# Kernel optimization log

Hardware: AMD Instinct MI355X
Metric: run time of the kernel (lower is better)

Reference implementation:

```python
import jax, jax.numpy as jnp
import numpy as np

SCALE_REACH = 10.0   # 'scale' in forward
SCALE_COS = 16.0     # CosNorm_Classifier default scale


def setup_inputs() -> dict:
    key = jax.random.key(0)
    ks = jax.random.split(key, 7)
    B, C, F = 64, 1000, 2048
    return {
        "x": jax.random.normal(ks[0], (B, F), jnp.float32),
        "centroids": jax.random.normal(ks[1], (C, F), jnp.float32),
        "W_hall": jax.random.normal(ks[2], (C, F), jnp.float32) * 0.02,
        "b_hall": jax.random.normal(ks[3], (C,), jnp.float32) * 0.02,
        "W_sel": jax.random.normal(ks[4], (F, F), jnp.float32) * 0.02,
        "b_sel": jax.random.normal(ks[5], (F,), jnp.float32) * 0.02,
        "W_cos": jax.random.normal(ks[6], (C, F), jnp.float32) * 0.001,
    }


def reference(x, centroids, W_hall, b_hall, W_sel, b_sel, W_cos):
    direct_feature = x
    # L2 distance to every class centroid: [B, C] (materializes [B, C, F] diff as in torch)
    diff = x[:, None, :] - centroids[None, :, :]
    dist = jnp.sqrt(jnp.sum(diff * diff, axis=2))
    # original sorts then takes column 0 -> min distance
    min_dist = jnp.min(dist, axis=1)                      # [B]
    reachability = (SCALE_REACH / min_dist)[:, None]      # [B, 1], broadcast over feat

    # hallucinated memory read
    values_memory = jax.nn.softmax(x @ W_hall.T + b_hall, axis=1)  # [B, C]
    memory_feature = values_memory @ centroids                      # [B, F]

    concept_selector = jnp.tanh(x @ W_sel.T + b_sel)                # [B, F]
    infused_feature = concept_selector * memory_feature
    feat = reachability * (direct_feature + infused_feature)

    # CosNorm classifier
    norm_x = jnp.linalg.norm(feat, axis=1, keepdims=True)           # [B, 1]
    ex = (norm_x / (1.0 + norm_x)) * (feat / norm_x)                # norm-gated unit vec
    ew = W_cos / jnp.linalg.norm(W_cos, axis=1, keepdims=True)      # [C, F]
    logits = ex @ (ew.T * SCALE_COS)                                # [B, C]

    return logits, direct_feature, infused_feature
```

## Files before the change

kernel.cpp:

```cpp
#include <hip/hip_runtime.h>
#include <math.h>

#define FF 2048

typedef __attribute__((ext_vector_type(8))) short short8;
typedef __attribute__((ext_vector_type(4))) float floatx4;

#define OFF_SPART 0
#define OFF_HPART 512000
#define OFF_SELP  1024000
#define OFF_MEMP  2072576
#define OFF_LOGP  3121152
#define OFF_V     4145152
#define OFF_FEAT  4210688
#define OFF_CN2   4341760
#define OFF_WINV  4342760
#define OFF_XN2   4343760
#define OFF_REACH 4343824
#define OFF_NRM2P 4343888

#define TP 40

__device__ __forceinline__ void split2(float f, ushort& h, ushort& l) {
  unsigned u = __float_as_uint(f);
  float r = f - __uint_as_float(u & 0xffff0000u);
  h = (ushort)(u >> 16);
  l = (ushort)(__float_as_uint(r) >> 16);
}

__device__ __forceinline__ void stage_bt_bf(const float* __restrict__ M, int ldK, int rowBase,
                                            int nrows, int k0, int kmax,
                                            ushort* __restrict__ hi, ushort* __restrict__ lo, int t) {
  int r = t >> 2, q = t & 3;
  int grow = rowBase + r;
  bool rok = grow < nrows;
  const float* src = M + (size_t)grow * ldK + k0 + q * 8;
#pragma unroll
  for (int h = 0; h < 2; ++h) {
    int kb = k0 + q * 8 + h * 4;
    float4 v = make_float4(0.f, 0.f, 0.f, 0.f);
    if (rok) {
      if (kb + 3 < kmax) {
        v = *(const float4*)(src + h * 4);
      } else {
#pragma unroll
        for (int j = 0; j < 4; ++j)
          if (kb + j < kmax) ((float*)&v)[j] = src[h * 4 + j];
      }
    }
    ushort4 hv, lv;
    split2(v.x, hv.x, lv.x); split2(v.y, hv.y, lv.y);
    split2(v.z, hv.z, lv.z); split2(v.w, hv.w, lv.w);
    int base = r * TP + q * 8 + h * 4;
    *(ushort4*)(hi + base) = hv;
    *(ushort4*)(lo + base) = lv;
  }
}

__device__ __forceinline__ void stage_tr_bf(const float* __restrict__ M, int ldN, int k0, int kmax,
                                            int n0, ushort* __restrict__ hi, ushort* __restrict__ lo, int t) {
  int kk = t >> 3, c8 = (t & 7) * 8;
  int gk = k0 + kk;
  const float* src = M + (size_t)gk * ldN + n0 + c8;
  float4 v0 = make_float4(0.f, 0.f, 0.f, 0.f), v1 = v0;
  if (gk < kmax) { v0 = *(const float4*)src; v1 = *(const float4*)(src + 4); }
#pragma unroll
  for (int j = 0; j < 8; ++j) {
    float f = (j < 4) ? ((float*)&v0)[j] : ((float*)&v1)[j - 4];
    ushort h, l;
    split2(f, h, l);
    hi[(c8 + j) * TP + kk] = h;
    lo[(c8 + j) * TP + kk] = l;
  }
}

#define MFMA(a, b, c) __builtin_amdgcn_mfma_f32_16x16x32_bf16(a, b, c, 0, 0, 0)

__global__ __launch_bounds__(256) void ka_gemm1(
    const float* __restrict__ x, const float* __restrict__ cent,
    const float* __restrict__ whall, const float* __restrict__ wsel,
    const float* __restrict__ wcos, float* __restrict__ ws) {
  __shared__ __align__(16) ushort u_lds[6 * 64 * TP];
  ushort* Ah  = u_lds;
  ushort* Al  = u_lds + 64 * TP;
  ushort* B1h = u_lds + 2 * 64 * TP;
  ushort* B1l = u_lds + 3 * 64 * TP;
  ushort* B2h = u_lds + 4 * 64 * TP;
  ushort* B2l = u_lds + 5 * 64 * TP;
  int bx = blockIdx.x, t = threadIdx.x;
  int lane = t & 63, w = t >> 6;
  int ln15 = t & 15, lq = (t >> 4) & 3, q8 = lq * 8;
  int mh = w & 1, nh = w >> 1;

  for (int r = bx * 4 + w; r < 2064; r += 2048) {
    const float* src = (r < 1000) ? cent + (size_t)r * FF
                     : (r < 2000) ? wcos + (size_t)(r - 1000) * FF
                                  : x + (size_t)(r - 2000) * FF;
    float s = 0.f;
#pragma unroll
    for (int i = 0; i < 8; ++i) {
      float4 v = *(const float4*)(src + i * 256 + lane * 4);
      s += v.x * v.x + v.y * v.y + v.z * v.z + v.w * v.w;
    }
#pragma unroll
    for (int off = 32; off > 0; off >>= 1) s += __shfl_down(s, off, 64);
    if (lane == 0) {
      if (r < 1000) ws[OFF_CN2 + r] = s;
      else if (r < 2000) ws[OFF_WINV + (r - 1000)] = 1.f / sqrtf(s);
      else ws[OFF_XN2 + (r - 2000)] = s;
    }
  }

  if (bx < 128) {
    int tile = bx & 15, ks = bx >> 4;
    int n0 = tile * 64;
    floatx4 accS[2][2], accH[2][2];
#pragma unroll
    for (int i = 0; i < 2; ++i)
#pragma unroll
      for (int j = 0; j < 2; ++j) { accS[i][j] = (floatx4){0.f,0.f,0.f,0.f}; accH[i][j] = (floatx4){0.f,0.f,0.f,0.f}; }
    for (int kc = 0; kc < 8; ++kc) {
      int k0 = ks * 256 + kc * 32;
      __syncthreads();
      stage_bt_bf(x,     FF, 0,  64,   k0, FF, Ah,  Al,  t);
      stage_bt_bf(cent,  FF, n0, 1000, k0, FF, B1h, B1l, t);
      stage_bt_bf(whall, FF, n0, 1000, k0, FF, B2h, B2l, t);
      __syncthreads();
      short8 ah[2], al[2];
#pragma unroll
      for (int i = 0; i < 2; ++i) {
        int row = (mh * 2 + i) * 16 + ln15;
        ah[i] = *(const short8*)(Ah + row * TP + q8);
        al[i] = *(const short8*)(Al + row * TP + q8);
      }
#pragma unroll
      for (int j = 0; j < 2; ++j) {
        int brow = (nh * 2 + j) * 16 + ln15;
        short8 b1h = *(const short8*)(B1h + brow * TP + q8);
        short8 b1l = *(const short8*)(B1l + brow * TP + q8);
        short8 b2h = *(const short8*)(B2h + brow * TP + q8);
        short8 b2l = *(const short8*)(B2l + brow * TP + q8);
#pragma unroll
        for (int i = 0; i < 2; ++i) {
          accS[i][j] = MFMA(ah[i], b1h, accS[i][j]);
          accS[i][j] = MFMA(ah[i], b1l, accS[i][j]);
          accS[i][j] = MFMA(al[i], b1h, accS[i][j]);
          accH[i][j] = MFMA(ah[i], b2h, accH[i][j]);
          accH[i][j] = MFMA(ah[i], b2l, accH[i][j]);
          accH[i][j] = MFMA(al[i], b2h, accH[i][j]);
        }
      }
    }
    float* Spart = ws + OFF_SPART + (size_t)ks * 64000;
    float* Hpart = ws + OFF_HPART + (size_t)ks * 64000;
#pragma unroll
    for (int i = 0; i < 2; ++i)
#pragma unroll
      for (int j = 0; j < 2; ++j) {
        int gn = n0 + (nh * 2 + j) * 16 + ln15;
        if (gn < 1000) {
#pragma unroll
          for (int r = 0; r < 4; ++r) {
            int gm = (mh * 2 + i) * 16 + lq * 4 + r;
            Spart[gm * 1000 + gn] = accS[i][j][r];
            Hpart[gm * 1000 + gn] = accH[i][j][r];
          }
        }
      }
  } else if (bx < 384) {
    int b2 = bx - 128;
    int tile = b2 & 31, ks = b2 >> 5;
    int n0 = tile * 64;
    floatx4 acc[2][2];
#pragma unroll
    for (int i = 0; i < 2; ++i)
#pragma unroll
      for (int j = 0; j < 2; ++j) acc[i][j] = (floatx4){0.f,0.f,0.f,0.f};
    for (int kc = 0; kc < 8; ++kc) {
      int k0 = ks * 256 + kc * 32;
      __syncthreads();
      stage_bt_bf(x,    FF, 0,  64, k0, FF, Ah,  Al,  t);
      stage_bt_bf(wsel, FF, n0, FF, k0, FF, B1h, B1l, t);
      __syncthreads();
      short8 ah[2], al[2];
#pragma unroll
      for (int i = 0; i < 2; ++i) {
        int row = (mh * 2 + i) * 16 + ln15;
        ah[i] = *(const short8*)(Ah + row * TP + q8);
        al[i] = *(const short8*)(Al + row * TP + q8);
      }
#pragma unroll
      for (int j = 0; j < 2; ++j) {
        int brow = (nh * 2 + j) * 16 + ln15;
        short8 bh = *(const short8*)(B1h + brow * TP + q8);
        short8 bl = *(const short8*)(B1l + brow * TP + q8);
#pragma unroll
        for (int i = 0; i < 2; ++i) {
          acc[i][j] = MFMA(ah[i], bh, acc[i][j]);
          acc[i][j] = MFMA(ah[i], bl, acc[i][j]);
          acc[i][j] = MFMA(al[i], bh, acc[i][j]);
        }
      }
    }
    float* selp = ws + OFF_SELP + (size_t)ks * 131072;
#pragma unroll
    for (int i = 0; i < 2; ++i)
#pragma unroll
      for (int j = 0; j < 2; ++j) {
        int gn = n0 + (nh * 2 + j) * 16 + ln15;
#pragma unroll
        for (int r = 0; r < 4; ++r) {
          int gm = (mh * 2 + i) * 16 + lq * 4 + r;
          selp[gm * 2048 + gn] = acc[i][j][r];
        }
      }
  }
}

__global__ __launch_bounds__(256) void kb_softmax(const float* __restrict__ bhall,
                                                  float* __restrict__ ws) {
  __shared__ float hrow[1000];
  __shared__ float red[256];
  int b = blockIdx.x, t = threadIdx.x;
  float xn = ws[OFF_XN2 + b];
  float lmin = 3.0e38f, lmax = -3.0e38f;
  if (t < 250) {
    int c0 = t * 4;
    floatx4 S = {0.f,0.f,0.f,0.f}, H = {0.f,0.f,0.f,0.f};
#pragma unroll
    for (int ks = 0; ks < 8; ++ks) {
      floatx4 sv = *(const floatx4*)(ws + OFF_SPART + (size_t)ks * 64000 + b * 1000 + c0);
      floatx4 hv = *(const floatx4*)(ws + OFF_HPART + (size_t)ks * 64000 + b * 1000 + c0);
      S += sv; H += hv;
    }
    floatx4 bh = *(const floatx4*)(bhall + c0);
    floatx4 cn = *(const floatx4*)(ws + OFF_CN2 + c0);
#pragma unroll
    for (int j = 0; j < 4; ++j) {
      float Hf = H[j] + bh[j];
      hrow[c0 + j] = Hf;
      float d2 = xn - 2.f * S[j] + cn[j];
      lmin = fminf(lmin, d2);
      lmax = fmaxf(lmax, Hf);
    }
  }
  red[t] = lmin; __syncthreads();
  for (int s = 128; s > 0; s >>= 1) { if (t < s) red[t] = fminf(red[t], red[t + s]); __syncthreads(); }
  float bmin = red[0]; __syncthreads();
  red[t] = lmax; __syncthreads();
  for (int s = 128; s > 0; s >>= 1) { if (t < s) red[t] = fmaxf(red[t], red[t + s]); __syncthreads(); }
  float bmax = red[0]; __syncthreads();
  float lsum = 0.f;
  float e4[4] = {0.f, 0.f, 0.f, 0.f};
  if (t < 250) {
#pragma unroll
    for (int j = 0; j < 4; ++j) {
      e4[j] = expf(hrow[t * 4 + j] - bmax);
      lsum += e4[j];
    }
  }
  red[t] = lsum; __syncthreads();
  for (int s = 128; s > 0; s >>= 1) { if (t < s) red[t] += red[t + s]; __syncthreads(); }
  float inv = 1.f / red[0];
  if (t < 250)
    *(floatx4*)(ws + OFF_V + b * 1024 + t * 4) =
        (floatx4){e4[0] * inv, e4[1] * inv, e4[2] * inv, e4[3] * inv};
  if (t == 250) {
#pragma unroll
    for (int j = 0; j < 24; ++j) ws[OFF_V + b * 1024 + 1000 + j] = 0.f;
  }
  if (t == 0) ws[OFF_REACH + b] = 10.f / sqrtf(bmin);
}

__global__ __launch_bounds__(256) void kc_mem(const float* __restrict__ cent,
                                              float* __restrict__ ws) {
  __shared__ __align__(16) ushort u_lds[4 * 64 * TP];
  ushort* Ah  = u_lds;
  ushort* Al  = u_lds + 64 * TP;
  ushort* B1h = u_lds + 2 * 64 * TP;
  ushort* B1l = u_lds + 3 * 64 * TP;
  int bx = blockIdx.x, t = threadIdx.x;
  int tile = bx & 31, ks = bx >> 5;
  int n0 = tile * 64;
  int ln15 = t & 15, lq = (t >> 4) & 3, q8 = lq * 8;
  int w = t >> 6, mh = w & 1, nh = w >> 1;
  const float* V = ws + OFF_V;
  floatx4 acc[2][2];
#pragma unroll
  for (int i = 0; i < 2; ++i)
#pragma unroll
    for (int j = 0; j < 2; ++j) acc[i][j] = (floatx4){0.f,0.f,0.f,0.f};
  for (int kc = 0; kc < 4; ++kc) {
    int k0 = ks * 128 + kc * 32;
    __syncthreads();
    {
      int r = t >> 2, q = t & 3;
#pragma unroll
      for (int h = 0; h < 2; ++h) {
        float4 v = *(const float4*)(V + (size_t)r * 1024 + k0 + q * 8 + h * 4);
        ushort4 hv, lv;
        split2(v.x, hv.x, lv.x); split2(v.y, hv.y, lv.y);
        split2(v.z, hv.z, lv.z); split2(v.w, hv.w, lv.w);
        int base = r * TP + q * 8 + h * 4;
        *(ushort4*)(Ah + base) = hv;
        *(ushort4*)(Al + base) = lv;
      }
    }
    stage_tr_bf(cent, FF, k0, 1000, n0, B1h, B1l, t);
    __syncthreads();
    short8 ah[2], al[2];
#pragma unroll
    for (int i = 0; i < 2; ++i) {
      int row = (mh * 2 + i) * 16 + ln15;
      ah[i] = *(const short8*)(Ah + row * TP + q8);
      al[i] = *(const short8*)(Al + row * TP + q8);
    }
#pragma unroll
    for (int j = 0; j < 2; ++j) {
      int brow = (nh * 2 + j) * 16 + ln15;
      short8 bh = *(const short8*)(B1h + brow * TP + q8);
      short8 bl = *(const short8*)(B1l + brow * TP + q8);
#pragma unroll
      for (int i = 0; i < 2; ++i) {
        acc[i][j] = MFMA(ah[i], bh, acc[i][j]);
        acc[i][j] = MFMA(ah[i], bl, acc[i][j]);
        acc[i][j] = MFMA(al[i], bh, acc[i][j]);
      }
    }
  }
  float* memp = ws + OFF_MEMP + (size_t)ks * 131072;
#pragma unroll
  for (int i = 0; i < 2; ++i)
#pragma unroll
    for (int j = 0; j < 2; ++j) {
      int gn = n0 + (nh * 2 + j) * 16 + ln15;
#pragma unroll
      for (int r = 0; r < 4; ++r) {
        int gm = (mh * 2 + i) * 16 + lq * 4 + r;
        memp[gm * 2048 + gn] = acc[i][j][r];
      }
    }
}

__global__ __launch_bounds__(64) void kd_fuse(const float* __restrict__ x,
                                              const float* __restrict__ bsel,
                                              float* __restrict__ ws, float* __restrict__ out) {
  int bx = blockIdx.x, t = threadIdx.x;
  int row = bx >> 3, ch = bx & 7;
  int f = ch * 256 + t * 4;
  const float* selp = ws + OFF_SELP + (size_t)row * 2048 + f;
  const float* memp = ws + OFF_MEMP + (size_t)row * 2048 + f;
  floatx4 sp = {0.f,0.f,0.f,0.f}, mm = {0.f,0.f,0.f,0.f};
#pragma unroll
  for (int ks = 0; ks < 8; ++ks) {
    sp += *(const floatx4*)(selp + (size_t)ks * 131072);
    mm += *(const floatx4*)(memp + (size_t)ks * 131072);
  }
  float4 bs4 = *(const float4*)(bsel + f);
  float4 x4  = *(const float4*)(x + (size_t)row * 2048 + f);
  float rch = ws[OFF_REACH + row];
  float4 inf4;
  floatx4 ft4;
  float nrm2 = 0.f;
#pragma unroll
  for (int j = 0; j < 4; ++j) {
    float sel = tanhf(sp[j] + ((float*)&bs4)[j]);
    float inf = sel * mm[j];
    float ft = rch * (((float*)&x4)[j] + inf);
    ((float*)&inf4)[j] = inf;
    ft4[j] = ft;
    nrm2 += ft * ft;
  }
  *(float4*)(out + 64000 + (size_t)row * 2048 + f) = x4;
  *(float4*)(out + 195072 + (size_t)row * 2048 + f) = inf4;
  *(floatx4*)(ws + OFF_FEAT + (size_t)row * 2048 + f) = ft4;
#pragma unroll
  for (int off = 32; off > 0; off >>= 1) nrm2 += __shfl_down(nrm2, off, 64);
  if (t == 0) ws[OFF_NRM2P + row * 8 + ch] = nrm2;
}

__global__ __launch_bounds__(256) void ke_logits(const float* __restrict__ wcos,
                                                 float* __restrict__ ws) {
  __shared__ __align__(16) ushort u_lds[4 * 64 * TP];
  ushort* Ah  = u_lds;
  ushort* Al  = u_lds + 64 * TP;
  ushort* B1h = u_lds + 2 * 64 * TP;
  ushort* B1l = u_lds + 3 * 64 * TP;
  int bx = blockIdx.x, t = threadIdx.x;
  int tile = bx & 15, ks = bx >> 4;
  int n0 = tile * 64;
  int ln15 = t & 15, lq = (t >> 4) & 3, q8 = lq * 8;
  int w = t >> 6, mh = w & 1, nh = w >> 1;
  const float* feat = ws + OFF_FEAT;
  floatx4 acc[2][2];
#pragma unroll
  for (int i = 0; i < 2; ++i)
#pragma unroll
    for (int j = 0; j < 2; ++j) acc[i][j] = (floatx4){0.f,0.f,0.f,0.f};
  for (int kc = 0; kc < 4; ++kc) {
    int k0 = ks * 128 + kc * 32;
    __syncthreads();
    {
      int r = t >> 2, q = t & 3;
#pragma unroll
      for (int h = 0; h < 2; ++h) {
        float4 v = *(const float4*)(feat + (size_t)r * 2048 + k0 + q * 8 + h * 4);
        ushort4 hv, lv;
        split2(v.x, hv.x, lv.x); split2(v.y, hv.y, lv.y);
        split2(v.z, hv.z, lv.z); split2(v.w, hv.w, lv.w);
        int base = r * TP + q * 8 + h * 4;
        *(ushort4*)(Ah + base) = hv;
        *(ushort4*)(Al + base) = lv;
      }
    }
    stage_bt_bf(wcos, FF, n0, 1000, k0, FF, B1h, B1l, t);
    __syncthreads();
    short8 ah[2], al[2];
#pragma unroll
    for (int i = 0; i < 2; ++i) {
      int row = (mh * 2 + i) * 16 + ln15;
      ah[i] = *(const short8*)(Ah + row * TP + q8);
      al[i] = *(const short8*)(Al + row * TP + q8);
    }
#pragma unroll
    for (int j = 0; j < 2; ++j) {
      int brow = (nh * 2 + j) * 16 + ln15;
      short8 bh = *(const short8*)(B1h + brow * TP + q8);
      short8 bl = *(const short8*)(B1l + brow * TP + q8);
#pragma unroll
      for (int i = 0; i < 2; ++i) {
        acc[i][j] = MFMA(ah[i], bh, acc[i][j]);
        acc[i][j] = MFMA(ah[i], bl, acc[i][j]);
        acc[i][j] = MFMA(al[i], bh, acc[i][j]);
      }
    }
  }
  float* logp = ws + OFF_LOGP + (size_t)ks * 64000;
#pragma unroll
  for (int i = 0; i < 2; ++i)
#pragma unroll
    for (int j = 0; j < 2; ++j) {
      int gn = n0 + (nh * 2 + j) * 16 + ln15;
      if (gn < 1000) {
#pragma unroll
        for (int r = 0; r < 4; ++r) {
          int gm = (mh * 2 + i) * 16 + lq * 4 + r;
          logp[gm * 1000 + gn] = acc[i][j][r];
        }
      }
    }
}

__global__ __launch_bounds__(128) void kf_final(float* __restrict__ ws, float* __restrict__ out) {
  int bx = blockIdx.x, t = threadIdx.x;
  int idx0 = (bx * 128 + t) * 4;
  const float* logp = ws + OFF_LOGP + idx0;
  floatx4 s = {0.f,0.f,0.f,0.f};
#pragma unroll
  for (int ks = 0; ks < 16; ++ks)
    s += *(const floatx4*)(logp + (size_t)ks * 64000);
  floatx4 o4;
  int pb = -1;
  float sfac = 0.f;
#pragma unroll
  for (int j = 0; j < 4; ++j) {
    int idx = idx0 + j;
    int bb = idx / 1000;
    int cc = idx - bb * 1000;
    if (bb != pb) {
      float n2 = 0.f;
#pragma unroll
      for (int q = 0; q < 8; ++q) n2 += ws[OFF_NRM2P + bb * 8 + q];
      sfac = 16.f / (1.f + sqrtf(n2));
      pb = bb;
    }
    o4[j] = s[j] * sfac * ws[OFF_WINV + cc];
  }
  *(floatx4*)(out + idx0) = o4;
}

extern "C" void kernel_launch(void* const* d_in, const int* in_sizes, int n_in,
                              void* d_out, int out_size, void* d_ws, size_t ws_size,
                              hipStream_t stream) {
  const float* x     = (const float*)d_in[0];
  const float* cent  = (const float*)d_in[1];
  const float* whall = (const float*)d_in[2];
  const float* bhall = (const float*)d_in[3];
  const float* wsel  = (const float*)d_in[4];
  const float* bsel  = (const float*)d_in[5];
  const float* wcos  = (const float*)d_in[6];
  float* out = (float*)d_out;
  float* ws  = (float*)d_ws;

  hipLaunchKernelGGL(ka_gemm1,   dim3(512), dim3(256), 0, stream, x, cent, whall, wsel, wcos, ws);
  hipLaunchKernelGGL(kb_softmax, dim3(64),  dim3(256), 0, stream, bhall, ws);
  hipLaunchKernelGGL(kc_mem,     dim3(256), dim3(256), 0, stream, cent, ws);
  hipLaunchKernelGGL(kd_fuse,    dim3(512), dim3(64),  0, stream, x, bsel, ws, out);
  hipLaunchKernelGGL(ke_logits,  dim3(256), dim3(256), 0, stream, wcos, ws);
  hipLaunchKernelGGL(kf_final,   dim3(125), dim3(128), 0, stream, ws, out);
}
```

Measured before the change: 131.6 us.

## Fuse six kernels into one cooperative persistent kernel with grid syncs

Replaces the six separate kernel launches with a single cooperative kernel of 512 blocks that runs every stage and separates them with grid.sync(). The first GEMM stage is rebalanced so each block handles a single B matrix (cent, whall or wsel) instead of some blocks doing two GEMMs at once, which spreads the work over all 512 blocks. This is meant to remove launch gaps and inter-kernel drain, at the cost of grid-wide barriers, idle blocks during the small stages, and the need for all 512 blocks to be co-resident (launch_bounds 256,2).

```diff
diff --git a/kernel.cpp b/kernel.cpp
--- a/kernel.cpp
+++ b/kernel.cpp
@@ -1,5 +1,8 @@
 #include <hip/hip_runtime.h>
+#include <hip/hip_cooperative_groups.h>
 #include <math.h>
+
+namespace cg = cooperative_groups;
 
 #define FF 2048
 
@@ -76,21 +79,22 @@
 
 #define MFMA(a, b, c) __builtin_amdgcn_mfma_f32_16x16x32_bf16(a, b, c, 0, 0, 0)
 
-__global__ __launch_bounds__(256) void ka_gemm1(
+__global__ __launch_bounds__(256, 2) void mega(
     const float* __restrict__ x, const float* __restrict__ cent,
-    const float* __restrict__ whall, const float* __restrict__ wsel,
-    const float* __restrict__ wcos, float* __restrict__ ws) {
-  __shared__ __align__(16) ushort u_lds[6 * 64 * TP];
-  ushort* Ah  = u_lds;
-  ushort* Al  = u_lds + 64 * TP;
-  ushort* B1h = u_lds + 2 * 64 * TP;
-  ushort* B1l = u_lds + 3 * 64 * TP;
-  ushort* B2h = u_lds + 4 * 64 * TP;
-  ushort* B2l = u_lds + 5 * 64 * TP;
-  int bx = blockIdx.x, t = threadIdx.x;
-  int lane = t & 63, w = t >> 6;
-  int ln15 = t & 15, lq = (t >> 4) & 3, q8 = lq * 8;
-  int mh = w & 1, nh = w >> 1;
+    const float* __restrict__ whall, const float* __restrict__ bhall,
+    const float* __restrict__ wsel, const float* __restrict__ bsel,
+    const float* __restrict__ wcos, float* __restrict__ ws,
+    float* __restrict__ out) {
+  cg::grid_group grid = cg::this_grid();
+  __shared__ __align__(16) ushort u_lds[4 * 64 * TP];
+  ushort* Ah = u_lds;
+  ushort* Al = u_lds + 64 * TP;
+  ushort* Bh = u_lds + 2 * 64 * TP;
+  ushort* Bl = u_lds + 3 * 64 * TP;
+  const int bx = blockIdx.x, t = threadIdx.x;
+  const int lane = t & 63, w = t >> 6;
+  const int ln15 = t & 15, lq = (t >> 4) & 3, q8 = lq * 8;
+  const int mh = w & 1, nh = w >> 1;
 
   for (int r = bx * 4 + w; r < 2064; r += 2048) {
     const float* src = (r < 1000) ? cent + (size_t)r * FF
@@ -111,20 +115,24 @@
     }
   }
 
-  if (bx < 128) {
-    int tile = bx & 15, ks = bx >> 4;
-    int n0 = tile * 64;
-    floatx4 accS[2][2], accH[2][2];
-#pragma unroll
-    for (int i = 0; i < 2; ++i)
-#pragma unroll
-      for (int j = 0; j < 2; ++j) { accS[i][j] = (floatx4){0.f,0.f,0.f,0.f}; accH[i][j] = (floatx4){0.f,0.f,0.f,0.f}; }
+  {
+    const int tile = bx & 63, ks = bx >> 6;
+    const float* Bm;
+    float* outp;
+    int n0, nB, ldo;
+    if (tile < 16)      { Bm = cent;  n0 = tile * 64;        nB = 1000; outp = ws + OFF_SPART + (size_t)ks * 64000;  ldo = 1000; }
+    else if (tile < 32) { Bm = whall; n0 = (tile - 16) * 64; nB = 1000; outp = ws + OFF_HPART + (size_t)ks * 64000;  ldo = 1000; }
+    else                { Bm = wsel;  n0 = (tile - 32) * 64; nB = 2048; outp = ws + OFF_SELP  + (size_t)ks * 131072; ldo = 2048; }
+    floatx4 acc[2][2];
+#pragma unroll
+    for (int i = 0; i < 2; ++i)
+#pragma unroll
+      for (int j = 0; j < 2; ++j) acc[i][j] = (floatx4){0.f, 0.f, 0.f, 0.f};
     for (int kc = 0; kc < 8; ++kc) {
       int k0 = ks * 256 + kc * 32;
       __syncthreads();
-      stage_bt_bf(x,     FF, 0,  64,   k0, FF, Ah,  Al,  t);
-      stage_bt_bf(cent,  FF, n0, 1000, k0, FF, B1h, B1l, t);
-      stage_bt_bf(whall, FF, n0, 1000, k0, FF, B2h, B2l, t);
+      stage_bt_bf(x,  FF, 0,  64, k0, FF, Ah, Al, t);
+      stage_bt_bf(Bm, FF, n0, nB, k0, FF, Bh, Bl, t);
       __syncthreads();
       short8 ah[2], al[2];
 #pragma unroll
@@ -136,51 +144,116 @@
 #pragma unroll
       for (int j = 0; j < 2; ++j) {
         int brow = (nh * 2 + j) * 16 + ln15;
-        short8 b1h = *(const short8*)(B1h + brow * TP + q8);
-        short8 b1l = *(const short8*)(B1l + brow * TP + q8);
-        short8 b2h = *(const short8*)(B2h + brow * TP + q8);
-        short8 b2l = *(const short8*)(B2l + brow * TP + q8);
+        short8 bh = *(const short8*)(Bh + brow * TP + q8);
+        short8 bl = *(const short8*)(Bl + brow * TP + q8);
 #pragma unroll
         for (int i = 0; i < 2; ++i) {
-          accS[i][j] = MFMA(ah[i], b1h, accS[i][j]);
-          accS[i][j] = MFMA(ah[i], b1l, accS[i][j]);
-          accS[i][j] = MFMA(al[i], b1h, accS[i][j]);
-          accH[i][j] = MFMA(ah[i], b2h, accH[i][j]);
-          accH[i][j] = MFMA(ah[i], b2l, accH[i][j]);
-          accH[i][j] = MFMA(al[i], b2h, accH[i][j]);
-        }
-      }
-    }
-    float* Spart = ws + OFF_SPART + (size_t)ks * 64000;
-    float* Hpart = ws + OFF_HPART + (size_t)ks * 64000;
+          acc[i][j] = MFMA(ah[i], bh, acc[i][j]);
+          acc[i][j] = MFMA(ah[i], bl, acc[i][j]);
+          acc[i][j] = MFMA(al[i], bh, acc[i][j]);
+        }
+      }
+    }
 #pragma unroll
     for (int i = 0; i < 2; ++i)
 #pragma unroll
       for (int j = 0; j < 2; ++j) {
         int gn = n0 + (nh * 2 + j) * 16 + ln15;
-        if (gn < 1000) {
+        if (gn < nB) {
 #pragma unroll
           for (int r = 0; r < 4; ++r) {
             int gm = (mh * 2 + i) * 16 + lq * 4 + r;
-            Spart[gm * 1000 + gn] = accS[i][j][r];
-            Hpart[gm * 1000 + gn] = accH[i][j][r];
+            outp[gm * ldo + gn] = acc[i][j][r];
           }
         }
       }
-  } else if (bx < 384) {
-    int b2 = bx - 128;
-    int tile = b2 & 31, ks = b2 >> 5;
-    int n0 = tile * 64;
+  }
+
+  grid.sync();
+
+  if (bx < 64) {
+    float* fl = (float*)u_lds;
+    float* hrow = fl;
+    float* red = fl + 1024;
+    int b = bx;
+    float xn = ws[OFF_XN2 + b];
+    float lmin = 3.0e38f, lmax = -3.0e38f;
+    if (t < 250) {
+      int c0 = t * 4;
+      floatx4 S = {0.f, 0.f, 0.f, 0.f}, H = {0.f, 0.f, 0.f, 0.f};
+#pragma unroll
+      for (int ks = 0; ks < 8; ++ks) {
+        floatx4 sv = *(const floatx4*)(ws + OFF_SPART + (size_t)ks * 64000 + b * 1000 + c0);
+        floatx4 hv = *(const floatx4*)(ws + OFF_HPART + (size_t)ks * 64000 + b * 1000 + c0);
+        S += sv; H += hv;
+      }
+      floatx4 bh = *(const floatx4*)(bhall + c0);
+      floatx4 cn = *(const floatx4*)(ws + OFF_CN2 + c0);
+#pragma unroll
+      for (int j = 0; j < 4; ++j) {
+        float Hf = H[j] + bh[j];
+        hrow[c0 + j] = Hf;
+        float d2 = xn - 2.f * S[j] + cn[j];
+        lmin = fminf(lmin, d2);
+        lmax = fmaxf(lmax, Hf);
+      }
+    }
+    red[t] = lmin; __syncthreads();
+    for (int s = 128; s > 0; s >>= 1) { if (t < s) red[t] = fminf(red[t], red[t + s]); __syncthreads(); }
+    float bmin = red[0]; __syncthreads();
+    red[t] = lmax; __syncthreads();
+    for (int s = 128; s > 0; s >>= 1) { if (t < s) red[t] = fmaxf(red[t], red[t + s]); __syncthreads(); }
+    float bmax = red[0]; __syncthreads();
+    float lsum = 0.f;
+    float e4[4] = {0.f, 0.f, 0.f, 0.f};
+    if (t < 250) {
+#pragma unroll
+      for (int j = 0; j < 4; ++j) {
+        e4[j] = expf(hrow[t * 4 + j] - bmax);
+        lsum += e4[j];
+      }
+    }
+    red[t] = lsum; __syncthreads();
+    for (int s = 128; s > 0; s >>= 1) { if (t < s) red[t] += red[t + s]; __syncthreads(); }
+    float inv = 1.f / red[0];
+    if (t < 250)
+      *(floatx4*)(ws + OFF_V + b * 1024 + t * 4) =
+          (floatx4){e4[0] * inv, e4[1] * inv, e4[2] * inv, e4[3] * inv};
+    if (t == 250) {
+#pragma unroll
+      for (int j = 0; j < 24; ++j) ws[OFF_V + b * 1024 + 1000 + j] = 0.f;
+    }
+    if (t == 0) ws[OFF_REACH + b] = 10.f / sqrtf(bmin);
+  }
+
+  grid.sync();
+
+  if (bx < 256) {
+    const int tile = bx & 31, ks = bx >> 5;
+    const int n0 = tile * 64;
+    const float* V = ws + OFF_V;
     floatx4 acc[2][2];
 #pragma unroll
     for (int i = 0; i < 2; ++i)
 #pragma unroll
-      for (int j = 0; j < 2; ++j) acc[i][j] = (floatx4){0.f,0.f,0.f,0.f};
-    for (int kc = 0; kc < 8; ++kc) {
-      int k0 = ks * 256 + kc * 32;
-      __syncthreads();
-      stage_bt_bf(x,    FF, 0,  64, k0, FF, Ah,  Al,  t);
-      stage_bt_bf(wsel, FF, n0, FF, k0, FF, B1h, B1l, t);
+      for (int j = 0; j < 2; ++j) acc[i][j] = (floatx4){0.f, 0.f, 0.f, 0.f};
+    for (int kc = 0; kc < 4; ++kc) {
+      int k0 = ks * 128 + kc * 32;
+      __syncthreads();
+      {
+        int r = t >> 2, q = t & 3;
+#pragma unroll
+        for (int h = 0; h < 2; ++h) {
+          float4 v = *(const float4*)(V + (size_t)r * 1024 + k0 + q * 8 + h * 4);
+          ushort4 hv, lv;
+          split2(v.x, hv.x, lv.x); split2(v.y, hv.y, lv.y);
+          split2(v.z, hv.z, lv.z); split2(v.w, hv.w, lv.w);
+          int base = r * TP + q * 8 + h * 4;
+          *(ushort4*)(Ah + base) = hv;
+          *(ushort4*)(Al + base) = lv;
+        }
+      }
+      stage_tr_bf(cent, FF, k0, 1000, n0, Bh, Bl, t);
       __syncthreads();
       short8 ah[2], al[2];
 #pragma unroll
@@ -192,8 +265,8 @@
 #pragma unroll
       for (int j = 0; j < 2; ++j) {
         int brow = (nh * 2 + j) * 16 + ln15;
-        short8 bh = *(const short8*)(B1h + brow * TP + q8);
-        short8 bl = *(const short8*)(B1l + brow * TP + q8);
+        short8 bh = *(const short8*)(Bh + brow * TP + q8);
+        short8 bl = *(const short8*)(Bl + brow * TP + q8);
 #pragma unroll
         for (int i = 0; i < 2; ++i) {
           acc[i][j] = MFMA(ah[i], bh, acc[i][j]);
@@ -202,7 +275,7 @@
         }
       }
     }
-    float* selp = ws + OFF_SELP + (size_t)ks * 131072;
+    float* memp = ws + OFF_MEMP + (size_t)ks * 131072;
 #pragma unroll
     for (int i = 0; i < 2; ++i)
 #pragma unroll
@@ -211,272 +284,142 @@
 #pragma unroll
         for (int r = 0; r < 4; ++r) {
           int gm = (mh * 2 + i) * 16 + lq * 4 + r;
-          selp[gm * 2048 + gn] = acc[i][j][r];
-        }
-      }
-  }
-}
-
-__global__ __launch_bounds__(256) void kb_softmax(const float* __restrict__ bhall,
-                                                  float* __restrict__ ws) {
-  __shared__ float hrow[1000];
-  __shared__ float red[256];
-  int b = blockIdx.x, t = threadIdx.x;
-  float xn = ws[OFF_XN2 + b];
-  float lmin = 3.0e38f, lmax = -3.0e38f;
-  if (t < 250) {
-    int c0 = t * 4;
-    floatx4 S = {0.f,0.f,0.f,0.f}, H = {0.f,0.f,0.f,0.f};
+          memp[gm * 2048 + gn] = acc[i][j][r];
+        }
+      }
+  }
+
+  grid.sync();
+
+  if (bx < 128) {
+    int row = bx >> 1, half = bx & 1;
+    int f = half * 1024 + t * 4;
+    const float* selp = ws + OFF_SELP + (size_t)row * 2048 + f;
+    const float* memp = ws + OFF_MEMP + (size_t)row * 2048 + f;
+    floatx4 sp = {0.f, 0.f, 0.f, 0.f}, mm = {0.f, 0.f, 0.f, 0.f};
 #pragma unroll
     for (int ks = 0; ks < 8; ++ks) {
-      floatx4 sv = *(const floatx4*)(ws + OFF_SPART + (size_t)ks * 64000 + b * 1000 + c0);
-      floatx4 hv = *(const floatx4*)(ws + OFF_HPART + (size_t)ks * 64000 + b * 1000 + c0);
-      S += sv; H += hv;
-    }
-    floatx4 bh = *(const floatx4*)(bhall + c0);
-    floatx4 cn = *(const floatx4*)(ws + OFF_CN2 + c0);
+      sp += *(const floatx4*)(selp + (size_t)ks * 131072);
+      mm += *(const floatx4*)(memp + (size_t)ks * 131072);
+    }
+    float4 bs4 = *(const float4*)(bsel + f);
+    float4 x4  = *(const float4*)(x + (size_t)row * 2048 + f);
+    float rch = ws[OFF_REACH + row];
+    float4 inf4;
+    floatx4 ft4;
+    float nrm2 = 0.f;
 #pragma unroll
     for (int j = 0; j < 4; ++j) {
-      float Hf = H[j] + bh[j];
-      hrow[c0 + j] = Hf;
-      float d2 = xn - 2.f * S[j] + cn[j];
-      lmin = fminf(lmin, d2);
-      lmax = fmaxf(lmax, Hf);
-    }
-  }
-  red[t] = lmin; __syncthreads();
-  for (int s = 128; s > 0; s >>= 1) { if (t < s) red[t] = fminf(red[t], red[t + s]); __syncthreads(); }
-  float bmin = red[0]; __syncthreads();
-  red[t] = lmax; __syncthreads();
-  for (int s = 128; s > 0; s >>= 1) { if (t < s) red[t] = fmaxf(red[t], red[t + s]); __syncthreads(); }
-  float bmax = red[0]; __syncthreads();
-  float lsum = 0.f;
-  float e4[4] = {0.f, 0.f, 0.f, 0.f};
-  if (t < 250) {
-#pragma unroll
-    for (int j = 0; j < 4; ++j) {
-      e4[j] = expf(hrow[t * 4 + j] - bmax);
-      lsum += e4[j];
-    }
-  }
-  red[t] = lsum; __syncthreads();
-  for (int s = 128; s > 0; s >>= 1) { if (t < s) red[t] += red[t + s]; __syncthreads(); }
-  float inv = 1.f / red[0];
-  if (t < 250)
-    *(floatx4*)(ws + OFF_V + b * 1024 + t * 4) =
-        (floatx4){e4[0] * inv, e4[1] * inv, e4[2] * inv, e4[3] * inv};
-  if (t == 250) {
-#pragma unroll
-    for (int j = 0; j < 24; ++j) ws[OFF_V + b * 1024 + 1000 + j] = 0.f;
-  }
-  if (t == 0) ws[OFF_REACH + b] = 10.f / sqrtf(bmin);
-}
-
-__global__ __launch_bounds__(256) void kc_mem(const float* __restrict__ cent,
-                                              float* __restrict__ ws) {
-  __shared__ __align__(16) ushort u_lds[4 * 64 * TP];
-  ushort* Ah  = u_lds;
-  ushort* Al  = u_lds + 64 * TP;
-  ushort* B1h = u_lds + 2 * 64 * TP;
-  ushort* B1l = u_lds + 3 * 64 * TP;
-  int bx = blockIdx.x, t = threadIdx.x;
-  int tile = bx & 31, ks = bx >> 5;
-  int n0 = tile * 64;
-  int ln15 = t & 15, lq = (t >> 4) & 3, q8 = lq * 8;
-  int w = t >> 6, mh = w & 1, nh = w >> 1;
-  const float* V = ws + OFF_V;
-  floatx4 acc[2][2];
-#pragma unroll
-  for (int i = 0; i < 2; ++i)
-#pragma unroll
-    for (int j = 0; j < 2; ++j) acc[i][j] = (floatx4){0.f,0.f,0.f,0.f};
-  for (int kc = 0; kc < 4; ++kc) {
-    int k0 = ks * 128 + kc * 32;
-    __syncthreads();
-    {
-      int r = t >> 2, q = t & 3;
-#pragma unroll
-      for (int h = 0; h < 2; ++h) {
-        float4 v = *(const float4*)(V + (size_t)r * 1024 + k0 + q * 8 + h * 4);
-        ushort4 hv, lv;
-        split2(v.x, hv.x, lv.x); split2(v.y, hv.y, lv.y);
-        split2(v.z, hv.z, lv.z); split2(v.w, hv.w, lv.w);
-        int base = r * TP + q * 8 + h * 4;
-        *(ushort4*)(Ah + base) = hv;
-        *(ushort4*)(Al + base) = lv;
-      }
-    }
-    stage_tr_bf(cent, FF, k0, 1000, n0, B1h, B1l, t);
-    __syncthreads();
-    short8 ah[2], al[2];
-#pragma unroll
-    for (int i = 0; i < 2; ++i) {
-      int row = (mh * 2 + i) * 16 + ln15;
-      ah[i] = *(const short8*)(Ah + row * TP + q8);
-      al[i] = *(const short8*)(Al + row * TP + q8);
-    }
-#pragma unroll
-    for (int j = 0; j < 2; ++j) {
-      int brow = (nh * 2 + j) * 16 + ln15;
-      short8 bh = *(const short8*)(B1h + brow * TP + q8);
-      short8 bl = *(const short8*)(B1l + brow * TP + q8);
+      float sel = tanhf(sp[j] + ((float*)&bs4)[j]);
+      float inf = sel * mm[j];
+      float ft = rch * (((float*)&x4)[j] + inf);
+      ((float*)&inf4)[j] = inf;
+      ft4[j] = ft;
+      nrm2 += ft * ft;
+    }
+    *(float4*)(out + 64000 + (size_t)row * 2048 + f) = x4;
+    *(float4*)(out + 195072 + (size_t)row * 2048 + f) = inf4;
+    *(floatx4*)(ws + OFF_FEAT + (size_t)row * 2048 + f) = ft4;
+#pragma unroll
+    for (int off = 32; off > 0; off >>= 1) nrm2 += __shfl_down(nrm2, off, 64);
+    if (lane == 0) ws[OFF_NRM2P + row * 8 + half * 4 + w] = nrm2;
+  }
+
+  grid.sync();
+
+  if (bx < 256) {
+    const int tile = bx & 15, ks = bx >> 4;
+    const int n0 = tile * 64;
+    const float* feat = ws + OFF_FEAT;
+    floatx4 acc[2][2];
+#pragma unroll
+    for (int i = 0; i < 2; ++i)
+#pragma unroll
+      for (int j = 0; j < 2; ++j) acc[i][j] = (floatx4){0.f, 0.f, 0.f, 0.f};
+    for (int kc = 0; kc < 4; ++kc) {
+      int k0 = ks * 128 + kc * 32;
+      __syncthreads();
+      {
+        int r = t >> 2, q = t & 3;
+#pragma unroll
+        for (int h = 0; h < 2; ++h) {
+          float4 v = *(const float4*)(feat + (size_t)r * 2048 + k0 + q * 8 + h * 4);
+          ushort4 hv, lv;
+          split2(v.x, hv.x, lv.x); split2(v.y, hv.y, lv.y);
+          split2(v.z, hv.z, lv.z); split2(v.w, hv.w, lv.w);
+          int base = r * TP + q * 8 + h * 4;
+          *(ushort4*)(Ah + base) = hv;
+          *(ushort4*)(Al + base) = lv;
+        }
+      }
+      stage_bt_bf(wcos, FF, n0, 1000, k0, FF, Bh, Bl, t);
+      __syncthreads();
+      short8 ah[2], al[2];
 #pragma unroll
       for (int i = 0; i < 2; ++i) {
-        acc[i][j] = MFMA(ah[i], bh, acc[i][j]);
-        acc[i][j] = MFMA(ah[i], bl, acc[i][j]);
-        acc[i][j] = MFMA(al[i], bh, acc[i][j]);
-      }
-    }
-  }
-  float* memp = ws + OFF_MEMP + (size_t)ks * 131072;
-#pragma unroll
-  for (int i = 0; i < 2; ++i)
-#pragma unroll
-    for (int j = 0; j < 2; ++j) {
-      int gn = n0 + (nh * 2 + j) * 16 + ln15;
-#pragma unroll
-      for (int r = 0; r < 4; ++r) {
-        int gm = (mh * 2 + i) * 16 + lq * 4 + r;
-        memp[gm * 2048 + gn] = acc[i][j][r];
-      }
-    }
-}
-
-__global__ __launch_bounds__(64) void kd_fuse(const float* __restrict__ x,
-                                              const float* __restrict__ bsel,
-                                              float* __restrict__ ws, float* __restrict__ out) {
-  int bx = blockIdx.x, t = threadIdx.x;
-  int row = bx >> 3, ch = bx & 7;
-  int f = ch * 256 + t * 4;
-  const float* selp = ws + OFF_SELP + (size_t)row * 2048 + f;
-  const float* memp = ws + OFF_MEMP + (size_t)row * 2048 + f;
-  floatx4 sp = {0.f,0.f,0.f,0.f}, mm = {0.f,0.f,0.f,0.f};
-#pragma unroll
-  for (int ks = 0; ks < 8; ++ks) {
-    sp += *(const floatx4*)(selp + (size_t)ks * 131072);
-    mm += *(const floatx4*)(memp + (size_t)ks * 131072);
-  }
-  float4 bs4 = *(const float4*)(bsel + f);
-  float4 x4  = *(const float4*)(x + (size_t)row * 2048 + f);
-  float rch = ws[OFF_REACH + row];
-  float4 inf4;
-  floatx4 ft4;
-  float nrm2 = 0.f;
-#pragma unroll
-  for (int j = 0; j < 4; ++j) {
-    float sel = tanhf(sp[j] + ((float*)&bs4)[j]);
-    float inf = sel * mm[j];
-    float ft = rch * (((float*)&x4)[j] + inf);
-    ((float*)&inf4)[j] = inf;
-    ft4[j] = ft;
-    nrm2 += ft * ft;
-  }
-  *(float4*)(out + 64000 + (size_t)row * 2048 + f) = x4;
-  *(float4*)(out + 195072 + (size_t)row * 2048 + f) = inf4;
-  *(floatx4*)(ws + OFF_FEAT + (size_t)row * 2048 + f) = ft4;
-#pragma unroll
-  for (int off = 32; off > 0; off >>= 1) nrm2 += __shfl_down(nrm2, off, 64);
-  if (t == 0) ws[OFF_NRM2P + row * 8 + ch] = nrm2;
-}
-
-__global__ __launch_bounds__(256) void ke_logits(const float* __restrict__ wcos,
-                                                 float* __restrict__ ws) {
-  __shared__ __align__(16) ushort u_lds[4 * 64 * TP];
-  ushort* Ah  = u_lds;
-  ushort* Al  = u_lds + 64 * TP;
-  ushort* B1h = u_lds + 2 * 64 * TP;
-  ushort* B1l = u_lds + 3 * 64 * TP;
-  int bx = blockIdx.x, t = threadIdx.x;
-  int tile = bx & 15, ks = bx >> 4;
-  int n0 = tile * 64;
-  int ln15 = t & 15, lq = (t >> 4) & 3, q8 = lq * 8;
-  int w = t >> 6, mh = w & 1, nh = w >> 1;
-  const float* feat = ws + OFF_FEAT;
-  floatx4 acc[2][2];
-#pragma unroll
-  for (int i = 0; i < 2; ++i)
-#pragma unroll
-    for (int j = 0; j < 2; ++j) acc[i][j] = (floatx4){0.f,0.f,0.f,0.f};
-  for (int kc = 0; kc < 4; ++kc) {
-    int k0 = ks * 128 + kc * 32;
-    __syncthreads();
-    {
-      int r = t >> 2, q = t & 3;
-#pragma unroll
-      for (int h = 0; h < 2; ++h) {
-        float4 v = *(const float4*)(feat + (size_t)r * 2048 + k0 + q * 8 + h * 4);
-        ushort4 hv, lv;
-        split2(v.x, hv.x, lv.x); split2(v.y, hv.y, lv.y);
-        split2(v.z, hv.z, lv.z); split2(v.w, hv.w, lv.w);
-        int base = r * TP + q * 8 + h * 4;
-        *(ushort4*)(Ah + base) = hv;
-        *(ushort4*)(Al + base) = lv;
-      }
-    }
-    stage_bt_bf(wcos, FF, n0, 1000, k0, FF, B1h, B1l, t);
-    __syncthreads();
-    short8 ah[2], al[2];
-#pragma unroll
-    for (int i = 0; i < 2; ++i) {
-      int row = (mh * 2 + i) * 16 + ln15;
-      ah[i] = *(const short8*)(Ah + row * TP + q8);
-      al[i] = *(const short8*)(Al + row * TP + q8);
-    }
-#pragma unroll
-    for (int j = 0; j < 2; ++j) {
-      int brow = (nh * 2 + j) * 16 + ln15;
-      short8 bh = *(const short8*)(B1h + brow * TP + q8);
-      short8 bl = *(const short8*)(B1l + brow * TP + q8);
-#pragma unroll
-      for (int i = 0; i < 2; ++i) {
-        acc[i][j] = MFMA(ah[i], bh, acc[i][j]);
-        acc[i][j] = MFMA(ah[i], bl, acc[i][j]);
-        acc[i][j] = MFMA(al[i], bh, acc[i][j]);
-      }
-    }
-  }
-  float* logp = ws + OFF_LOGP + (size_t)ks * 64000;
-#pragma unroll
-  for (int i = 0; i < 2; ++i)
-#pragma unroll
-    for (int j = 0; j < 2; ++j) {
-      int gn = n0 + (nh * 2 + j) * 16 + ln15;
-      if (gn < 1000) {
-#pragma unroll
-        for (int r = 0; r < 4; ++r) {
-          int gm = (mh * 2 + i) * 16 + lq * 4 + r;
-          logp[gm * 1000 + gn] = acc[i][j][r];
-        }
-      }
-    }
-}
-
-__global__ __launch_bounds__(128) void kf_final(float* __restrict__ ws, float* __restrict__ out) {
-  int bx = blockIdx.x, t = threadIdx.x;
-  int idx0 = (bx * 128 + t) * 4;
-  const float* logp = ws + OFF_LOGP + idx0;
-  floatx4 s = {0.f,0.f,0.f,0.f};
-#pragma unroll
-  for (int ks = 0; ks < 16; ++ks)
-    s += *(const floatx4*)(logp + (size_t)ks * 64000);
-  floatx4 o4;
-  int pb = -1;
-  float sfac = 0.f;
-#pragma unroll
-  for (int j = 0; j < 4; ++j) {
-    int idx = idx0 + j;
-    int bb = idx / 1000;
-    int cc = idx - bb * 1000;
-    if (bb != pb) {
-      float n2 = 0.f;
-#pragma unroll
-      for (int q = 0; q < 8; ++q) n2 += ws[OFF_NRM2P + bb * 8 + q];
-      sfac = 16.f / (1.f + sqrtf(n2));
-      pb = bb;
-    }
-    o4[j] = s[j] * sfac * ws[OFF_WINV + cc];
-  }
-  *(floatx4*)(out + idx0) = o4;
+        int row = (mh * 2 + i) * 16 + ln15;
+        ah[i] = *(const short8*)(Ah + row * TP + q8);
+        al[i] = *(const short8*)(Al + row * TP + q8);
+      }
+#pragma unroll
+      for (int j = 0; j < 2; ++j) {
+        int brow = (nh * 2 + j) * 16 + ln15;
+        short8 bh = *(const short8*)(Bh + brow * TP + q8);
+        short8 bl = *(const short8*)(Bl + brow * TP + q8);
+#pragma unroll
+        for (int i = 0; i < 2; ++i) {
+          acc[i][j] = MFMA(ah[i], bh, acc[i][j]);
+          acc[i][j] = MFMA(ah[i], bl, acc[i][j]);
+          acc[i][j] = MFMA(al[i], bh, acc[i][j]);
+        }
+      }
+    }
+    float* logp = ws + OFF_LOGP + (size_t)ks * 64000;
+#pragma unroll
+    for (int i = 0; i < 2; ++i)
+#pragma unroll
+      for (int j = 0; j < 2; ++j) {
+        int gn = n0 + (nh * 2 + j) * 16 + ln15;
+        if (gn < 1000) {
+#pragma unroll
+          for (int r = 0; r < 4; ++r) {
+            int gm = (mh * 2 + i) * 16 + lq * 4 + r;
+            logp[gm * 1000 + gn] = acc[i][j][r];
+          }
+        }
+      }
+  }
+
+  grid.sync();
+
+  {
+    int idx0 = (bx * 256 + t) * 4;
+    if (idx0 < 64000) {
+      const float* logp = ws + OFF_LOGP + idx0;
+      floatx4 s = {0.f, 0.f, 0.f, 0.f};
+#pragma unroll
+      for (int ks = 0; ks < 16; ++ks)
+        s += *(const floatx4*)(logp + (size_t)ks * 64000);
+      floatx4 o4;
+      int pb = -1;
+      float sfac = 0.f;
+#pragma unroll
+      for (int j = 0; j < 4; ++j) {
+        int idx = idx0 + j;
+        int bb = idx / 1000;
+        int cc = idx - bb * 1000;
+        if (bb != pb) {
+          float n2 = 0.f;
+#pragma unroll
+          for (int q = 0; q < 8; ++q) n2 += ws[OFF_NRM2P + bb * 8 + q];
+          sfac = 16.f / (1.f + sqrtf(n2));
+          pb = bb;
+        }
+        o4[j] = s[j] * sfac * ws[OFF_WINV + cc];
+      }
+      *(floatx4*)(out + idx0) = o4;
+    }
+  }
 }
 
 extern "C" void kernel_launch(void* const* d_in, const int* in_sizes, int n_in,
@@ -492,10 +435,7 @@
   float* out = (float*)d_out;
   float* ws  = (float*)d_ws;
 
-  hipLaunchKernelGGL(ka_gemm1,   dim3(512), dim3(256), 0, stream, x, cent, whall, wsel, wcos, ws);
-  hipLaunchKernelGGL(kb_softmax, dim3(64),  dim3(256), 0, stream, bhall, ws);
-  hipLaunchKernelGGL(kc_mem,     dim3(256), dim3(256), 0, stream, cent, ws);
-  hipLaunchKernelGGL(kd_fuse,    dim3(512), dim3(64),  0, stream, x, bsel, ws, out);
-  hipLaunchKernelGGL(ke_logits,  dim3(256), dim3(256), 0, stream, wcos, ws);
-  hipLaunchKernelGGL(kf_final,   dim3(125), dim3(128), 0, stream, ws, out);
+  void* args[] = {(void*)&x, (void*)&cent, (void*)&whall, (void*)&bhall,
+                  (void*)&wsel, (void*)&bsel, (void*)&wcos, (void*)&ws, (void*)&out};
+  hipLaunchCooperativeKernel((void*)mega, dim3(512), dim3(256), args, 0, stream);
 }
```

New measurement: 431.6 us. 3.28x slower.
